# Optimization experiments

Hardware: AMD Instinct MI355X
Metric: run time of the kernel (lower is better)

The kernel has to match this reference:

```python
import jax, jax.numpy as jnp
import numpy as np

V, C, TCTX, H, L = 32000, 768, 1024, 12, 6
B, T = 2, 1024
D = C // H
EPS = 1e-5


def setup_inputs() -> dict:
    key = jax.random.key(0)
    ks = jax.random.split(key, 12)
    s = lambda k, shape: jax.random.normal(k, shape, jnp.float32) * 0.02
    return {
        "x_indices": jax.random.randint(ks[0], (B, T), 0, V, jnp.int32),
        "tok_emb": s(ks[1], (V, C)),
        "pos_emb": s(ks[2], (TCTX, C)),
        "ln1_g": jnp.ones((L, C)), "ln1_b": jnp.zeros((L, C)),
        "wq": s(ks[3], (L, C, C)), "wk": s(ks[4], (L, C, C)), "wv": s(ks[5], (L, C, C)),
        "wo": s(ks[6], (L, C, C)), "bo": jnp.zeros((L, C)),
        "ln2_g": jnp.ones((L, C)), "ln2_b": jnp.zeros((L, C)),
        "w1": s(ks[7], (L, C, 4 * C)), "b1": jnp.zeros((L, 4 * C)),
        "w2": s(ks[8], (L, 4 * C, C)), "b2": jnp.zeros((L, C)),
        "lnf_g": jnp.ones((C,)), "lnf_b": jnp.zeros((C,)),
        "wp": s(ks[9], (C, V)), "bp": jnp.zeros((V,)),
    }


def _ln(x, g, b):
    m = x.mean(-1, keepdims=True)
    v = ((x - m) ** 2).mean(-1, keepdims=True)
    return (x - m) * jax.lax.rsqrt(v + EPS) * g + b


def _forward(x_indices, tok_emb, pos_emb, ln1_g, ln1_b, wq, wk, wv, wo, bo,
             ln2_g, ln2_b, w1, b1, w2, b2, lnf_g, lnf_b, wp, bp):
    Bv, Tv = x_indices.shape
    x = tok_emb[x_indices] + pos_emb[:Tv]  # [B,T,C]
    mask = jnp.tril(jnp.ones((Tv, Tv), dtype=bool))  # causal

    def block(x, p):
        g1, be1, q_w, k_w, v_w, o_w, o_b, g2, be2, f1, fb1, f2, fb2 = p
        h = _ln(x, g1, be1)
        q = (h @ q_w).reshape(Bv, Tv, H, D)
        k = (h @ k_w).reshape(Bv, Tv, H, D)
        v = (h @ v_w).reshape(Bv, Tv, H, D)
        scores = jnp.einsum('bthd,bshd->bhts', q, k) / jnp.sqrt(jnp.float32(D))
        scores = jnp.where(mask, scores, -jnp.inf)
        a = jax.nn.softmax(scores, axis=-1)
        o = jnp.einsum('bhts,bshd->bthd', a, v).reshape(Bv, Tv, C)
        x = x + o @ o_w + o_b
        h2 = _ln(x, g2, be2)
        x = x + jax.nn.relu(h2 @ f1 + fb1) @ f2 + fb2
        return x, None

    layer_params = (ln1_g, ln1_b, wq, wk, wv, wo, bo, ln2_g, ln2_b, w1, b1, w2, b2)
    x, _ = jax.lax.scan(block, x, layer_params)
    x = _ln(x, lnf_g, lnf_b)
    return x @ wp + bp  # logits [B,T,V]


def reference(x_indices, tok_emb, pos_emb, ln1_g, ln1_b, wq, wk, wv, wo, bo,
              ln2_g, ln2_b, w1, b1, w2, b2, lnf_g, lnf_b, wp, bp):
    return _forward(x_indices, tok_emb, pos_emb, ln1_g, ln1_b, wq, wk, wv, wo, bo,
                    ln2_g, ln2_b, w1, b1, w2, b2, lnf_g, lnf_b, wp, bp)
```

## Files before the change

kernel.cpp:

```cpp
#include <hip/hip_runtime.h>
#include <stdint.h>

#define DEV __device__ __forceinline__

typedef unsigned short u16;
typedef __attribute__((ext_vector_type(8))) short short8;
typedef __attribute__((ext_vector_type(4))) float floatx4;

#define B_ 2
#define T_ 1024
#define C_ 768
#define H_ 12
#define L_ 6
#define V_ 32000
#define F_ 3072
#define M_ 2048
#define C3_ 2304

#define VMW(n) asm volatile("s_waitcnt vmcnt(" #n ")" ::: "memory")
#define LGKM0 asm volatile("s_waitcnt lgkmcnt(0)" ::: "memory")
#define SBAR __builtin_amdgcn_s_barrier()
#define SCHED0 __builtin_amdgcn_sched_barrier(0)

DEV u16 f2bf(float f) {
  unsigned int u; __builtin_memcpy(&u, &f, 4);
  u += 0x7FFFu + ((u >> 16) & 1u);
  return (u16)(u >> 16);
}

DEV void gload16(const void* g, void* l) {
  __builtin_amdgcn_global_load_lds(
      (__attribute__((address_space(1))) void*)(uintptr_t)g,
      (__attribute__((address_space(3))) void*)(unsigned int)(uintptr_t)l,
      16, 0, 0);
}

DEV int xcd_swz(int flat, int nwg) {
  int q = nwg >> 3, r = nwg & 7;
  int xcd = flat & 7, sid = flat >> 3;
  return (xcd < r ? xcd * (q + 1) : r * (q + 1) + (xcd - r) * q) + sid;
}

__global__ __launch_bounds__(256) void transpose_f32_bf16(
    const float* __restrict__ src, u16* __restrict__ dst, int R, int Cc,
    size_t src_z, size_t dst_z) {
  __shared__ float tile[32][33];
  const float* s = src + (size_t)blockIdx.z * src_z;
  u16* d = dst + (size_t)blockIdx.z * dst_z;
  int c0 = blockIdx.x * 32, r0 = blockIdx.y * 32;
  int tx = threadIdx.x & 31, ty = threadIdx.x >> 5;
#pragma unroll
  for (int i = 0; i < 4; i++)
    tile[ty + 8 * i][tx] = s[(size_t)(r0 + ty + 8 * i) * Cc + (c0 + tx)];
  __syncthreads();
#pragma unroll
  for (int i = 0; i < 4; i++)
    d[(size_t)(c0 + ty + 8 * i) * R + (r0 + tx)] = f2bf(tile[tx][ty + 8 * i]);
}

__global__ __launch_bounds__(256) void embed_kernel(
    const int* __restrict__ idx, const float* __restrict__ tok,
    const float* __restrict__ pos, float* __restrict__ x) {
  int row = blockIdx.x;
  int t = row & (T_ - 1);
  int tk = idx[row];
  const float* tp = tok + (size_t)tk * C_;
  const float* pp = pos + (size_t)t * C_;
  float* xp = x + (size_t)row * C_;
  for (int c = threadIdx.x; c < C_; c += 256) xp[c] = tp[c] + pp[c];
}

__global__ __launch_bounds__(256) void ln_kernel(
    const float* __restrict__ x, const float* __restrict__ g,
    const float* __restrict__ b, u16* __restrict__ out) {
  int row = blockIdx.x;
  int tid = threadIdx.x;
  const float* xp = x + (size_t)row * C_;
  float v0 = xp[tid], v1 = xp[tid + 256], v2 = xp[tid + 512];
  float s = v0 + v1 + v2;
  float ss = v0 * v0 + v1 * v1 + v2 * v2;
#pragma unroll
  for (int o = 32; o > 0; o >>= 1) { s += __shfl_down(s, o); ss += __shfl_down(ss, o); }
  __shared__ float red[8];
  int wid = tid >> 6;
  if ((tid & 63) == 0) { red[wid] = s; red[4 + wid] = ss; }
  __syncthreads();
  float tot = red[0] + red[1] + red[2] + red[3];
  float tss = red[4] + red[5] + red[6] + red[7];
  float mean = tot * (1.f / C_);
  float var = tss * (1.f / C_) - mean * mean;
  float rstd = rsqrtf(var + 1e-5f);
  u16* op = out + (size_t)row * C_;
  op[tid]       = f2bf((v0 - mean) * rstd * g[tid]       + b[tid]);
  op[tid + 256] = f2bf((v1 - mean) * rstd * g[tid + 256] + b[tid + 256]);
  op[tid + 512] = f2bf((v2 - mean) * rstd * g[tid + 512] + b[tid + 512]);
}

template <int THREADS, int BM, int BN, int WM, int WN, int BIAS, int RELU, int OUTMODE, int SPLITK>
__global__ __launch_bounds__(THREADS) void gemm3(
    const u16* __restrict__ A, const u16* __restrict__ BT,
    const float* __restrict__ bias,
    u16* __restrict__ ob, float* __restrict__ fout, u16* __restrict__ vt,
    int N, int K) {
  constexpr int ALOADS = (BM * 64) / (THREADS * 16);
  constexpr int BLOADS = (BN * 64) / (THREADS * 16);
  constexpr int LDS_L = ALOADS + BLOADS;
  constexpr int MF = BM / (WM * 16);
  constexpr int NF = BN / (WN * 16);
  __shared__ __align__(16) u16 As[3][BM * 32];
  __shared__ __align__(16) u16 Bs[3][BN * 32];

  int tid = threadIdx.x;
  int lane = tid & 63, w = tid >> 6;
  int wm = w / WN, wn = w % WN;
  int rr = lane & 15, qg = lane >> 4;

  int gx = gridDim.x;
  int nwg = gx * gridDim.y;
  int flat = blockIdx.y * gx + blockIdx.x;
  int wg = xcd_swz(flat, nwg);
  int m0 = (wg % gx) * BM, n0 = (wg / gx) * BN;

  int kz = SPLITK > 1 ? blockIdx.z : 0;
  int Keff = SPLITK > 1 ? (K / SPLITK) : K;
  int kbase = kz * Keff;

  const u16* Aps[ALOADS];
  const u16* Bps[BLOADS];
#pragma unroll
  for (int i = 0; i < ALOADS; i++) {
    int idx = i * THREADS + tid;
    int row = idx >> 2;
    int chunk = (idx & 3) ^ ((row >> 1) & 3);
    Aps[i] = A + (size_t)(m0 + row) * K + chunk * 8 + kbase;
  }
#pragma unroll
  for (int i = 0; i < BLOADS; i++) {
    int idx = i * THREADS + tid;
    int row = idx >> 2;
    int chunk = (idx & 3) ^ ((row >> 1) & 3);
    Bps[i] = BT + (size_t)(n0 + row) * K + chunk * 8 + kbase;
  }

  auto stage = [&](int sl, int kk) {
#pragma unroll
    for (int i = 0; i < ALOADS; i++)
      gload16(Aps[i] + kk, (char*)As + (size_t)sl * BM * 64 + i * THREADS * 16 + w * 1024);
#pragma unroll
    for (int i = 0; i < BLOADS; i++)
      gload16(Bps[i] + kk, (char*)Bs + (size_t)sl * BN * 64 + i * THREADS * 16 + w * 1024);
  };

  floatx4 zero = {0.f, 0.f, 0.f, 0.f};
  floatx4 acc[MF][NF];
#pragma unroll
  for (int i = 0; i < MF; i++)
#pragma unroll
    for (int j = 0; j < NF; j++) acc[i][j] = zero;

  int NT = Keff >> 5;
  stage(0, 0);
  stage(1, 32);
  if constexpr (LDS_L == 2) VMW(2);
  else if constexpr (LDS_L == 3) VMW(3);
  else if constexpr (LDS_L == 4) VMW(4);
  else VMW(6);
  SBAR;
  SCHED0;

  int sqA = (qg ^ ((rr >> 1) & 3)) << 4;

  for (int t = 0; t < NT; ++t) {
    int sl = t % 3;
    if (t + 2 < NT) stage((t + 2) % 3, (t + 2) << 5);
    SCHED0;
    const char* Ab = (const char*)As + (size_t)sl * BM * 64;
    const char* Bb = (const char*)Bs + (size_t)sl * BN * 64;
    short8 af[MF], bf[NF];
#pragma unroll
    for (int i = 0; i < MF; i++)
      af[i] = *(const short8*)(Ab + ((wm * (BM / WM) + i * 16 + rr) << 6) + sqA);
#pragma unroll
    for (int j = 0; j < NF; j++)
      bf[j] = *(const short8*)(Bb + ((wn * (BN / WN) + j * 16 + rr) << 6) + sqA);
    __builtin_amdgcn_s_setprio(1);
#pragma unroll
    for (int i = 0; i < MF; i++)
#pragma unroll
      for (int j = 0; j < NF; j++)
        acc[i][j] = __builtin_amdgcn_mfma_f32_16x16x32_bf16(af[i], bf[j], acc[i][j], 0, 0, 0);
    __builtin_amdgcn_s_setprio(0);
    if (t < NT - 2) {
      if constexpr (LDS_L == 2) VMW(2);
      else if constexpr (LDS_L == 3) VMW(3);
      else if constexpr (LDS_L == 4) VMW(4);
      else VMW(6);
    } else if (t == NT - 2) VMW(0);
    if (t < NT - 1) { SBAR; SCHED0; }
  }

  int cb = n0 + wn * (BN / WN);
  int rb = m0 + wm * (BM / WM);
  bool isv = (OUTMODE == 3) && (n0 >= 1536);
#pragma unroll
  for (int i = 0; i < MF; i++) {
#pragma unroll
    for (int j = 0; j < NF; j++) {
      int col = cb + j * 16 + rr;
      float bv = 0.f;
      if (BIAS && kz == 0) bv = bias[col];
      float vals[4];
#pragma unroll
      for (int r = 0; r < 4; r++) {
        float val = acc[i][j][r] + bv;
        if (RELU) val = fmaxf(val, 0.f);
        vals[r] = val;
      }
      int row0 = rb + i * 16 + qg * 4;
      if (isv) {
        int colv = col - 1536;
        int bb = row0 >> 10, t0 = row0 & (T_ - 1);
        uint2 pk;
        pk.x = (unsigned int)f2bf(vals[0]) | ((unsigned int)f2bf(vals[1]) << 16);
        pk.y = (unsigned int)f2bf(vals[2]) | ((unsigned int)f2bf(vals[3]) << 16);
        *(uint2*)&vt[((size_t)bb * C_ + colv) * T_ + t0] = pk;
      } else {
#pragma unroll
        for (int r = 0; r < 4; r++) {
          size_t o = (size_t)(row0 + r) * N + col;
          if (OUTMODE == 0 || OUTMODE == 3) ob[o] = f2bf(vals[r]);
          else if (OUTMODE == 1) {
            if (SPLITK > 1) atomicAdd(&fout[o], vals[r]);
            else fout[o] += vals[r];
          } else fout[o] = vals[r];
        }
      }
    }
  }
}

__global__ __launch_bounds__(512) void gemm8(
    const u16* __restrict__ A, const u16* __restrict__ BT,
    const float* __restrict__ bias, float* __restrict__ fout, int N, int K) {
  __shared__ __align__(16) u16 As[2][2][128 * 64];
  __shared__ __align__(16) u16 Bs[2][2][128 * 64];
  int tid = threadIdx.x;
  int lane = tid & 63, w = tid >> 6;
  int wr = w >> 2, wc = w & 3;
  int rr = lane & 15, qg = lane >> 4;

  int gx = gridDim.x;
  int nwg = gx * gridDim.y;
  int flat = blockIdx.y * gx + blockIdx.x;
  int wg = xcd_swz(flat, nwg);
  int m0 = (wg % gx) * 256, n0 = (wg / gx) * 256;

  int la = tid >> 3;
  int sa = (((tid & 7) ^ (la & 7)) << 3);
  const u16* Ap0 = A + (size_t)(m0 + la) * K + sa;
  const u16* Ap1 = A + (size_t)(m0 + 128 + la) * K + sa;
  int lb0 = la, lb1 = 64 + la;
  const u16* Bp0 = BT + (size_t)(n0 + (lb0 >> 5) * 64 + (lb0 & 31)) * K + sa;
  const u16* Bp1 = BT + (size_t)(n0 + (lb1 >> 5) * 64 + (lb1 & 31)) * K + sa;

  auto stA = [&](int buf, int mh, int kt) {
    size_t off = (size_t)mh * 64 * K + kt * 64;
    gload16(Ap0 + off, (char*)&As[buf][mh][0] + w * 1024);
    gload16(Ap1 + off, (char*)&As[buf][mh][0] + 8192 + w * 1024);
  };
  auto stB = [&](int buf, int nh, int kt) {
    size_t off = (size_t)nh * 32 * K + kt * 64;
    gload16(Bp0 + off, (char*)&Bs[buf][nh][0] + w * 1024);
    gload16(Bp1 + off, (char*)&Bs[buf][nh][0] + 8192 + w * 1024);
  };
  auto stageOrd = [&](int buf, int h, int kt) {
    if (h == 0) stA(buf, 0, kt);
    else if (h == 1) stB(buf, 0, kt);
    else if (h == 2) stB(buf, 1, kt);
    else stA(buf, 1, kt);
  };

  floatx4 zero = {0.f, 0.f, 0.f, 0.f};
  floatx4 acc[8][4];
#pragma unroll
  for (int i = 0; i < 8; i++)
#pragma unroll
    for (int j = 0; j < 4; j++) acc[i][j] = zero;

  short8 a[2][4], b[2][2];
  int NKT = K >> 6;
  int NIT = NKT >> 1;

  stageOrd(0, 0, 0); stageOrd(0, 1, 0); stageOrd(0, 2, 0); stageOrd(0, 3, 0);
  VMW(4);
  SBAR;
  SCHED0;

  for (int it = 0; it < NIT; ++it) {
    int kt2 = it * 2;
    bool last = (it == NIT - 1);
#pragma unroll
    for (int p = 0; p < 8; ++p) {
      const int d = p >> 2;
      const int q = p & 3;
      const int mh = q >> 1, nh = q & 1;
      const char* Abp = (const char*)&As[d][mh][0];
      const char* Bbp = (const char*)&Bs[d][nh][0];
      if (q == 0 || q == 2) {
#pragma unroll
        for (int kk = 0; kk < 2; kk++)
#pragma unroll
          for (int i = 0; i < 4; i++) {
            int l = wr * 64 + i * 16 + rr;
            a[kk][i] = *(const short8*)(Abp + l * 128 + ((((kk << 2) + qg) ^ (rr & 7)) << 4));
          }
      }
#pragma unroll
      for (int kk = 0; kk < 2; kk++)
#pragma unroll
        for (int j = 0; j < 2; j++) {
          int l = wc * 32 + j * 16 + rr;
          b[kk][j] = *(const short8*)(Bbp + l * 128 + ((((kk << 2) + qg) ^ (rr & 7)) << 4));
        }
      if (p < 4) stageOrd(1, q, kt2 + 1);
      else if (!last) stageOrd(0, q, kt2 + 2);
      SCHED0;
      SBAR;
      LGKM0;
      SCHED0;
      __builtin_amdgcn_s_setprio(1);
#pragma unroll
      for (int kk = 0; kk < 2; kk++)
#pragma unroll
        for (int i = 0; i < 4; i++)
#pragma unroll
          for (int j = 0; j < 2; j++)
            acc[mh * 4 + i][nh * 2 + j] = __builtin_amdgcn_mfma_f32_16x16x32_bf16(
                a[kk][i], b[kk][j], acc[mh * 4 + i][nh * 2 + j], 0, 0, 0);
      __builtin_amdgcn_s_setprio(0);
      if (!last || p < 4) VMW(4);
      else if (p == 4) VMW(2);
      else if (p == 5) VMW(0);
      SBAR;
      SCHED0;
    }
  }

  int rbase = m0 + wr * 128;
  int cbase = n0 + wc * 64;
#pragma unroll
  for (int fi = 0; fi < 8; fi++) {
    int row0 = rbase + (fi >> 2) * 64 + (fi & 3) * 16 + qg * 4;
#pragma unroll
    for (int fj = 0; fj < 4; fj++) {
      int col = cbase + (fj >> 1) * 32 + (fj & 1) * 16 + rr;
      float bv = bias[col];
#pragma unroll
      for (int r = 0; r < 4; r++)
        fout[(size_t)(row0 + r) * N + col] = acc[fi][fj][r] + bv;
    }
  }
}

__global__ __launch_bounds__(64) void attn_kernel(
    const u16* __restrict__ qkv, const u16* __restrict__ vt, u16* __restrict__ o) {
  __shared__ __align__(16) u16 P_s[16 * 48];
  int nwg = gridDim.x;
  int wg = xcd_swz(blockIdx.x, nwg);
  int qt = wg & 63;
  int h = (wg >> 6) % H_;
  int b = wg / (64 * H_);
  int q0 = qt << 4;
  int lane = threadIdx.x;
  int rr = lane & 15, qg = lane >> 4, kq = qg << 3;

  const u16* qb = qkv + (size_t)(b * T_ + q0 + rr) * C3_ + h * 64;
  short8 qf0 = *(const short8*)(qb + kq);
  short8 qf1 = *(const short8*)(qb + 32 + kq);

  float m_r = -1e30f, l_r = 0.f;
  floatx4 zero = {0.f, 0.f, 0.f, 0.f};
  floatx4 oacc[4];
#pragma unroll
  for (int d = 0; d < 4; d++) oacc[d] = zero;

  const u16* kbase = qkv + (size_t)(b * T_) * C3_ + 768 + h * 64;
  const u16* vbase = vt + (size_t)(b * C_ + h * 64) * T_;

  for (int kt0 = 0; kt0 <= q0 + 15; kt0 += 32) {
    floatx4 s[2];
#pragma unroll
    for (int c = 0; c < 2; c++) {
      const u16* kb = kbase + (size_t)(kt0 + c * 16 + rr) * C3_;
      short8 kf0 = *(const short8*)(kb + kq);
      short8 kf1 = *(const short8*)(kb + 32 + kq);
      floatx4 z = zero;
      z = __builtin_amdgcn_mfma_f32_16x16x32_bf16(kf0, qf0, z, 0, 0, 0);
      z = __builtin_amdgcn_mfma_f32_16x16x32_bf16(kf1, qf1, z, 0, 0, 0);
      s[c] = z;
    }
    int qpos = q0 + rr;
    float p[2][4];
    float mx = -1e30f;
#pragma unroll
    for (int c = 0; c < 2; c++)
#pragma unroll
      for (int r = 0; r < 4; r++) {
        int kpos = kt0 + c * 16 + qg * 4 + r;
        float val = s[c][r] * 0.125f;
        val = (kpos <= qpos) ? val : -1e30f;
        p[c][r] = val;
        mx = fmaxf(mx, val);
      }
    mx = fmaxf(mx, __shfl_xor(mx, 16));
    mx = fmaxf(mx, __shfl_xor(mx, 32));
    float mn = fmaxf(m_r, mx);
    float escL = exp2f((m_r - mn) * 1.44269504f);
    m_r = mn;
    float ps = 0.f;
#pragma unroll
    for (int c = 0; c < 2; c++)
#pragma unroll
      for (int r = 0; r < 4; r++) {
        float pv = exp2f((p[c][r] - mn) * 1.44269504f);
        p[c][r] = pv;
        ps += pv;
      }
    ps += __shfl_xor(ps, 16);
    ps += __shfl_xor(ps, 32);
    l_r = l_r * escL + ps;
#pragma unroll
    for (int c = 0; c < 2; c++) {
      unsigned int u0 = (unsigned int)f2bf(p[c][0]) | ((unsigned int)f2bf(p[c][1]) << 16);
      unsigned int u1 = (unsigned int)f2bf(p[c][2]) | ((unsigned int)f2bf(p[c][3]) << 16);
      uint2 pk; pk.x = u0; pk.y = u1;
      *(uint2*)&P_s[rr * 48 + c * 16 + qg * 4] = pk;
    }
    float er[4];
#pragma unroll
    for (int r = 0; r < 4; r++) er[r] = __shfl(escL, qg * 4 + r);
#pragma unroll
    for (int d = 0; d < 4; d++)
#pragma unroll
      for (int r = 0; r < 4; r++) oacc[d][r] *= er[r];
    short8 pa = *(const short8*)&P_s[rr * 48 + kq];
#pragma unroll
    for (int d = 0; d < 4; d++) {
      short8 vf = *(const short8*)(vbase + (size_t)(d * 16 + rr) * T_ + kt0 + kq);
      oacc[d] = __builtin_amdgcn_mfma_f32_16x16x32_bf16(pa, vf, oacc[d], 0, 0, 0);
    }
  }
  float lb[4];
#pragma unroll
  for (int r = 0; r < 4; r++) lb[r] = __shfl(l_r, qg * 4 + r);
  u16* obp = o + (size_t)(b * T_ + q0) * C_ + h * 64;
#pragma unroll
  for (int d = 0; d < 4; d++)
#pragma unroll
    for (int r = 0; r < 4; r++) {
      int row = qg * 4 + r;
      obp[(size_t)row * C_ + d * 16 + rr] = f2bf(oacc[d][r] / lb[r]);
    }
}

extern "C" void kernel_launch(void* const* d_in, const int* in_sizes, int n_in,
                              void* d_out, int out_size, void* d_ws, size_t ws_size,
                              hipStream_t stream) {
  (void)in_sizes; (void)n_in; (void)out_size; (void)ws_size;
  const int*   xidx = (const int*)d_in[0];
  const float* tok  = (const float*)d_in[1];
  const float* pos  = (const float*)d_in[2];
  const float* ln1g = (const float*)d_in[3];
  const float* ln1b = (const float*)d_in[4];
  const float* wq   = (const float*)d_in[5];
  const float* wk   = (const float*)d_in[6];
  const float* wv   = (const float*)d_in[7];
  const float* wo   = (const float*)d_in[8];
  const float* bo   = (const float*)d_in[9];
  const float* ln2g = (const float*)d_in[10];
  const float* ln2b = (const float*)d_in[11];
  const float* w1   = (const float*)d_in[12];
  const float* b1   = (const float*)d_in[13];
  const float* w2   = (const float*)d_in[14];
  const float* b2   = (const float*)d_in[15];
  const float* lnfg = (const float*)d_in[16];
  const float* lnfb = (const float*)d_in[17];
  const float* wp   = (const float*)d_in[18];
  const float* bp   = (const float*)d_in[19];

  char* ws = (char*)d_ws;
  size_t off = 0;
  auto alloc = [&](size_t bytes) { char* p = ws + off; off += (bytes + 255) & ~(size_t)255; return p; };
  u16* wqkvT = (u16*)alloc((size_t)L_ * 3 * C_ * C_ * 2);
  u16* woT = (u16*)alloc((size_t)L_ * C_ * C_ * 2);
  u16* w1T = (u16*)alloc((size_t)L_ * C_ * F_ * 2);
  u16* w2T = (u16*)alloc((size_t)L_ * C_ * F_ * 2);
  u16* wpT = (u16*)alloc((size_t)C_ * V_ * 2);
  float* x = (float*)alloc((size_t)M_ * C_ * 4);
  u16* hb   = (u16*)alloc((size_t)M_ * C_ * 2);
  u16* qkvb = (u16*)alloc((size_t)M_ * C3_ * 2);
  u16* vtb  = (u16*)alloc((size_t)M_ * C_ * 2);
  u16* aob  = (u16*)alloc((size_t)M_ * C_ * 2);
  u16* mb   = (u16*)alloc((size_t)M_ * F_ * 2);

  dim3 blk(256);
  size_t CC = (size_t)C_ * C_, CF = (size_t)C_ * F_;
  transpose_f32_bf16<<<dim3(C_ / 32, C_ / 32, L_), blk, 0, stream>>>(wq, wqkvT,          C_, C_, CC, 3 * CC);
  transpose_f32_bf16<<<dim3(C_ / 32, C_ / 32, L_), blk, 0, stream>>>(wk, wqkvT + CC,     C_, C_, CC, 3 * CC);
  transpose_f32_bf16<<<dim3(C_ / 32, C_ / 32, L_), blk, 0, stream>>>(wv, wqkvT + 2 * CC, C_, C_, CC, 3 * CC);
  transpose_f32_bf16<<<dim3(C_ / 32, C_ / 32, L_), blk, 0, stream>>>(wo, woT, C_, C_, CC, CC);
  transpose_f32_bf16<<<dim3(F_ / 32, C_ / 32, L_), blk, 0, stream>>>(w1, w1T, C_, F_, CF, CF);
  transpose_f32_bf16<<<dim3(C_ / 32, F_ / 32, L_), blk, 0, stream>>>(w2, w2T, F_, C_, CF, CF);
  transpose_f32_bf16<<<dim3(V_ / 32, C_ / 32, 1), blk, 0, stream>>>(wp, wpT, C_, V_, 0, 0);
  embed_kernel<<<M_, blk, 0, stream>>>(xidx, tok, pos, x);

  for (int l = 0; l < L_; ++l) {
    size_t wOff = (size_t)l * 3 * CC;
    size_t oOff = (size_t)l * CC;
    size_t fOff = (size_t)l * CF;
    ln_kernel<<<M_, blk, 0, stream>>>(x, ln1g + l * C_, ln1b + l * C_, hb);
    gemm3<256, 128, 128, 2, 2, 0, 0, 3, 1><<<dim3(M_ / 128, C3_ / 128), 256, 0, stream>>>(
        hb, wqkvT + wOff, nullptr, qkvb, nullptr, vtb, C3_, C_);
    attn_kernel<<<B_ * H_ * (T_ / 16), dim3(64), 0, stream>>>(qkvb, vtb, aob);
    gemm3<256, 128, 128, 2, 2, 1, 0, 1, 2><<<dim3(M_ / 128, C_ / 128, 2), 256, 0, stream>>>(
        aob, woT + oOff, bo + l * C_, nullptr, x, nullptr, C_, C_);
    ln_kernel<<<M_, blk, 0, stream>>>(x, ln2g + l * C_, ln2b + l * C_, hb);
    gemm3<256, 128, 128, 2, 2, 1, 1, 0, 1><<<dim3(M_ / 128, F_ / 128), 256, 0, stream>>>(
        hb, w1T + fOff, b1 + l * F_, mb, nullptr, nullptr, F_, C_);
    gemm3<256, 128, 128, 2, 2, 1, 0, 1, 2><<<dim3(M_ / 128, C_ / 128, 2), 256, 0, stream>>>(
        mb, w2T + fOff, b2 + l * C_, nullptr, x, nullptr, C_, F_);
  }
  ln_kernel<<<M_, blk, 0, stream>>>(x, lnfg, lnfb, hb);
  gemm8<<<dim3(M_ / 256, V_ / 256), 512, 0, stream>>>(
      hb, wpT, bp, (float*)d_out, V_, C_);
}
```

Measured before the change: 1.066 ms.

## Split attention KV loop across four waves with LDS softmax merge

The attention kernel now launches 256 threads per block, four wavefronts per 16-query tile. Each wave processes every fourth 32-key chunk, and waves 1-3 write their partial max, sum and output accumulators to shared memory. Wave 0 then merges them with online-softmax rescaling and writes the result. This shortens the serial KV loop per tile, which matters most for late query tiles with long causal ranges, at the cost of extra LDS, a barrier and a merge step. Waves with no chunk (early tiles) still contribute neutral partial state.

New measurement: 1.040 ms. 2.4% less time.

```diff
diff --git a/kernel.cpp b/kernel.cpp
--- a/kernel.cpp
+++ b/kernel.cpp
@@ -362,16 +362,20 @@
   }
 }
 
-__global__ __launch_bounds__(64) void attn_kernel(
+__global__ __launch_bounds__(256) void attn_kernel(
     const u16* __restrict__ qkv, const u16* __restrict__ vt, u16* __restrict__ o) {
-  __shared__ __align__(16) u16 P_s[16 * 48];
+  __shared__ __align__(16) u16 P_s[4][16 * 48];
+  __shared__ float mls[3][2][16];
+  __shared__ float osm[3][16][64];
   int nwg = gridDim.x;
   int wg = xcd_swz(blockIdx.x, nwg);
   int qt = wg & 63;
   int h = (wg >> 6) % H_;
   int b = wg / (64 * H_);
   int q0 = qt << 4;
-  int lane = threadIdx.x;
+  int tid = threadIdx.x;
+  int ws = tid >> 6;
+  int lane = tid & 63;
   int rr = lane & 15, qg = lane >> 4, kq = qg << 3;
 
   const u16* qb = qkv + (size_t)(b * T_ + q0 + rr) * C3_ + h * 64;
@@ -387,7 +391,7 @@
   const u16* kbase = qkv + (size_t)(b * T_) * C3_ + 768 + h * 64;
   const u16* vbase = vt + (size_t)(b * C_ + h * 64) * T_;
 
-  for (int kt0 = 0; kt0 <= q0 + 15; kt0 += 32) {
+  for (int kt0 = ws * 32; kt0 <= q0 + 15; kt0 += 128) {
     floatx4 s[2];
 #pragma unroll
     for (int c = 0; c < 2; c++) {
@@ -434,7 +438,7 @@
       unsigned int u0 = (unsigned int)f2bf(p[c][0]) | ((unsigned int)f2bf(p[c][1]) << 16);
       unsigned int u1 = (unsigned int)f2bf(p[c][2]) | ((unsigned int)f2bf(p[c][3]) << 16);
       uint2 pk; pk.x = u0; pk.y = u1;
-      *(uint2*)&P_s[rr * 48 + c * 16 + qg * 4] = pk;
+      *(uint2*)&P_s[ws][rr * 48 + c * 16 + qg * 4] = pk;
     }
     float er[4];
 #pragma unroll
@@ -443,24 +447,57 @@
     for (int d = 0; d < 4; d++)
 #pragma unroll
       for (int r = 0; r < 4; r++) oacc[d][r] *= er[r];
-    short8 pa = *(const short8*)&P_s[rr * 48 + kq];
+    short8 pa = *(const short8*)&P_s[ws][rr * 48 + kq];
 #pragma unroll
     for (int d = 0; d < 4; d++) {
       short8 vf = *(const short8*)(vbase + (size_t)(d * 16 + rr) * T_ + kt0 + kq);
       oacc[d] = __builtin_amdgcn_mfma_f32_16x16x32_bf16(pa, vf, oacc[d], 0, 0, 0);
     }
   }
-  float lb[4];
-#pragma unroll
-  for (int r = 0; r < 4; r++) lb[r] = __shfl(l_r, qg * 4 + r);
-  u16* obp = o + (size_t)(b * T_ + q0) * C_ + h * 64;
-#pragma unroll
-  for (int d = 0; d < 4; d++)
-#pragma unroll
-    for (int r = 0; r < 4; r++) {
-      int row = qg * 4 + r;
-      obp[(size_t)row * C_ + d * 16 + rr] = f2bf(oacc[d][r] / lb[r]);
-    }
+
+  if (ws != 0) {
+    if (qg == 0) { mls[ws - 1][0][rr] = m_r; mls[ws - 1][1][rr] = l_r; }
+#pragma unroll
+    for (int d = 0; d < 4; d++)
+#pragma unroll
+      for (int r = 0; r < 4; r++)
+        osm[ws - 1][qg * 4 + r][d * 16 + rr] = oacc[d][r];
+  }
+  __syncthreads();
+  if (ws == 0) {
+#pragma unroll
+    for (int s2 = 0; s2 < 3; s2++) {
+      float mw = mls[s2][0][rr];
+      float lw = mls[s2][1][rr];
+      float mn = fmaxf(m_r, mw);
+      float e0 = exp2f((m_r - mn) * 1.44269504f);
+      float e1 = exp2f((mw - mn) * 1.44269504f);
+      m_r = mn;
+      l_r = l_r * e0 + lw * e1;
+      float er0[4], er1[4];
+#pragma unroll
+      for (int r = 0; r < 4; r++) {
+        er0[r] = __shfl(e0, qg * 4 + r);
+        er1[r] = __shfl(e1, qg * 4 + r);
+      }
+#pragma unroll
+      for (int d = 0; d < 4; d++)
+#pragma unroll
+        for (int r = 0; r < 4; r++)
+          oacc[d][r] = oacc[d][r] * er0[r] + osm[s2][qg * 4 + r][d * 16 + rr] * er1[r];
+    }
+    float lb[4];
+#pragma unroll
+    for (int r = 0; r < 4; r++) lb[r] = __shfl(l_r, qg * 4 + r);
+    u16* obp = o + (size_t)(b * T_ + q0) * C_ + h * 64;
+#pragma unroll
+    for (int d = 0; d < 4; d++)
+#pragma unroll
+      for (int r = 0; r < 4; r++) {
+        int row = qg * 4 + r;
+        obp[(size_t)row * C_ + d * 16 + rr] = f2bf(oacc[d][r] / lb[r]);
+      }
+  }
 }
 
 extern "C" void kernel_launch(void* const* d_in, const int* in_sizes, int n_in,
@@ -521,7 +558,7 @@
     ln_kernel<<<M_, blk, 0, stream>>>(x, ln1g + l * C_, ln1b + l * C_, hb);
     gemm3<256, 128, 128, 2, 2, 0, 0, 3, 1><<<dim3(M_ / 128, C3_ / 128), 256, 0, stream>>>(
         hb, wqkvT + wOff, nullptr, qkvb, nullptr, vtb, C3_, C_);
-    attn_kernel<<<B_ * H_ * (T_ / 16), dim3(64), 0, stream>>>(qkvb, vtb, aob);
+    attn_kernel<<<B_ * H_ * (T_ / 16), dim3(256), 0, stream>>>(qkvb, vtb, aob);
     gemm3<256, 128, 128, 2, 2, 1, 0, 1, 2><<<dim3(M_ / 128, C_ / 128, 2), 256, 0, stream>>>(
         aob, woT + oOff, bo + l * C_, nullptr, x, nullptr, C_, C_);
     ln_kernel<<<M_, blk, 0, stream>>>(x, ln2g + l * C_, ln2b + l * C_, hb);
```
